# Kernel tuning notes

Hardware: AMD Instinct MI355X
Metric: run time of the kernel (lower is better)

The kernel has to match this reference:

```python
import jax, jax.numpy as jnp
import numpy as np

B, T = 4096, 512          # batch, max seq len
V, E, H, O = 57, 20, 128, 18  # vocab, embed, hidden, classes


def setup_inputs() -> dict:
    key = jax.random.key(0)
    ks = jax.random.split(key, 9)
    x = jax.random.randint(ks[0], (B, T), 0, V)
    lens = jax.random.randint(ks[1], (B,), 1, T + 1)
    x_lengths = jnp.sort(lens)[::-1]  # pack_padded_sequence needs descending lengths
    s = 1.0 / np.sqrt(H)
    emb = jax.random.normal(ks[2], (V, E), dtype=jnp.float32)
    W_ih = jax.random.uniform(ks[3], (H, E), minval=-s, maxval=s, dtype=jnp.float32)
    W_hh = jax.random.uniform(ks[4], (H, H), minval=-s, maxval=s, dtype=jnp.float32)
    b_ih = jax.random.uniform(ks[5], (H,), minval=-s, maxval=s, dtype=jnp.float32)
    b_hh = jax.random.uniform(ks[6], (H,), minval=-s, maxval=s, dtype=jnp.float32)
    so = 1.0 / np.sqrt(H)
    W_out = jax.random.uniform(ks[7], (O, H), minval=-so, maxval=so, dtype=jnp.float32)
    b_out = jax.random.uniform(ks[8], (O,), minval=-so, maxval=so, dtype=jnp.float32)
    return {"x": x, "x_lengths": x_lengths, "emb": emb, "W_ih": W_ih,
            "W_hh": W_hh, "b_ih": b_ih, "b_hh": b_hh, "W_out": W_out, "b_out": b_out}


def reference(x, x_lengths, emb, W_ih, W_hh, b_ih, b_hh, W_out, b_out):
    xe = emb[x]                                            # [B,T,E] embedding gather
    # precompute input projection + both biases once (hoisted out of recurrence)
    xw = jnp.einsum('bte,he->bth', xe, W_ih) + b_ih + b_hh  # [B,T,H]
    valid = jnp.arange(T)[None, :] < x_lengths[:, None]     # [B,T] packed-seq mask

    def step(h, inp):
        xw_t, v_t = inp                                     # [B,H], [B]
        h_new = jnp.tanh(xw_t + h @ W_hh.T)
        # packed RNN: stop updating once past this sequence's length,
        # so the final h equals the hidden state at step len-1
        h = jnp.where(v_t[:, None], h_new, h)
        return h, None

    h0 = jnp.zeros((B, H), dtype=xw.dtype)
    hT, _ = jax.lax.scan(step, h0, (jnp.swapaxes(xw, 0, 1), valid.T))  # scan over T
    logits = jax.nn.relu(hT) @ W_out.T + b_out              # [B,O]
    return jax.nn.log_softmax(logits, axis=1)
```

## Files before the change

kernel.cpp:

```cpp
#include <hip/hip_runtime.h>
#include <math.h>

#define Bn 4096
#define Tn 512
#define Vn 57
#define En 20
#define Hn 128
#define On 18
#define ROWS 16
#define NTHR 512
#define NBLK (Bn / ROWS)
#define KC 5
#define NKB 20
#define BUFH (NKB * 16 * 8)
#define ESTR 40
#define XSTR 513
#define HFSTR 132
#define ASCALE 2.8853900817779268f

typedef _Float16 half8  __attribute__((ext_vector_type(8)));
typedef _Float16 half4  __attribute__((ext_vector_type(4)));
typedef __fp16   fp16x2 __attribute__((ext_vector_type(2)));
typedef float    floatx4 __attribute__((ext_vector_type(4)));

__device__ __forceinline__ float tanh_scaled(float z) {
    float e = __builtin_amdgcn_exp2f(z);
    float r = __builtin_amdgcn_rcpf(e + 1.0f);
    return fmaf(-2.0f, r, 1.0f);
}

__device__ __forceinline__ unsigned pk_u32(fp16x2 v) {
    union { fp16x2 h; unsigned u; } c; c.h = v; return c.u;
}

__launch_bounds__(NTHR, 2)
__global__ void rnn_mfma_kernel(const int* __restrict__ x,
                                const int* __restrict__ xlen,
                                const float* __restrict__ emb,
                                const float* __restrict__ W_ih,
                                const float* __restrict__ W_hh,
                                const float* __restrict__ b_ih,
                                const float* __restrict__ b_hh,
                                const float* __restrict__ W_out,
                                const float* __restrict__ b_out,
                                float* __restrict__ out)
{
    __shared__ __align__(16) _Float16 sB[2][BUFH];
    __shared__ __align__(16) _Float16 sEmb[Vn * ESTR];
    __shared__ __align__(16) float    sHf[ROWS * HFSTR];
    __shared__ int sX[ROWS * XSTR];
    __shared__ float sLogit[ROWS][On];
    __shared__ float sMLS[ROWS];
    __shared__ float sPad[6200];

    const int tid  = threadIdx.x;
    const int blk  = blockIdx.x;
    const int row0 = blk * ROWS;

    ((volatile float*)sPad)[tid % 6200] = 0.0f;

    const int w    = tid >> 6;
    const int lane = tid & 63;
    const int n    = lane & 15;
    const int q    = lane >> 4;
    const bool stager = (w >= 4) && (lane < 16);
    const int  wk     = (w >= 4) ? (w - 4) : 0;

    half8 Ah[KC];
    #pragma unroll
    for (int kc = 0; kc < 4; ++kc) {
        const float* p = &W_hh[(16 * w + n) * Hn + kc * 32 + q * 8];
        #pragma unroll
        for (int i = 0; i < 8; ++i)
            Ah[kc][i] = (_Float16)(p[i] * ASCALE);
    }
    {
        #pragma unroll
        for (int i = 0; i < 8; ++i) {
            int e = q * 8 + i;
            float v = 0.0f;
            if (e < En)       v = W_ih[(16 * w + n) * En + e];
            else if (e == 20) v = b_ih[16 * w + n] + b_hh[16 * w + n];
            Ah[4][i] = (_Float16)(v * ASCALE);
        }
    }

    for (int idx = tid; idx < Vn * 32; idx += NTHR) {
        int c = idx >> 5, j = idx & 31;
        float v = (j < En) ? emb[c * En + j] : (j == 20 ? 1.0f : 0.0f);
        sEmb[c * ESTR + j] = (_Float16)v;
    }
    for (int idx = tid * 4; idx < ROWS * Tn; idx += NTHR * 4) {
        int4 v = *(const int4*)&x[row0 * Tn + idx];
        int r = idx >> 9, t = idx & 511;
        sX[r * XSTR + t]     = v.x;
        sX[r * XSTR + t + 1] = v.y;
        sX[r * XSTR + t + 2] = v.z;
        sX[r * XSTR + t + 3] = v.w;
    }
    for (int idx = tid; idx < 2 * BUFH / 8; idx += NTHR)
        ((float4*)sB)[idx] = make_float4(0.f, 0.f, 0.f, 0.f);
    __syncthreads();

    const int Lmax  = xlen[row0];
    const int len_n = xlen[row0 + n];

    if (stager) {
        int id0 = sX[lane * XSTR + 0];
        half8 xe0 = *(const half8*)&sEmb[id0 * ESTR + wk * 8];
        *(half8*)&sB[0][(16 + wk) * 128 + lane * 8] = xe0;
    }
    __syncthreads();

    float hreg[4] = {0.f, 0.f, 0.f, 0.f};

    const int bbase = q * 128 + n * 8;
    const int kbA   = 2 * w + (q >> 1);
    const int sadr  = kbA * 128 + n * 8 + 4 * (q & 1);

    int id_use = 0;
    if (stager) id_use = sX[lane * XSTR + (Lmax > 1 ? 1 : 0)];

    #define RNN_STEP(bp, np, t)                                                   \
    {                                                                             \
        half8 b[KC];                                                              \
        _Pragma("unroll")                                                         \
        for (int kc = 0; kc < KC; ++kc)                                           \
            b[kc] = *(const half8*)&(bp)[bbase + kc * 512];                       \
        half8 xe;                                                                 \
        int id_next = 0;                                                          \
        if (stager) {                                                             \
            xe = *(const half8*)&sEmb[id_use * ESTR + wk * 8];                    \
            id_next = sX[lane * XSTR + min((t) + 2, Lmax - 1)];                   \
        }                                                                         \
        floatx4 aE = {0.f, 0.f, 0.f, 0.f};                                        \
        floatx4 aO = {0.f, 0.f, 0.f, 0.f};                                        \
        aE = __builtin_amdgcn_mfma_f32_16x16x32_f16(Ah[0], b[0], aE, 0, 0, 0);    \
        aO = __builtin_amdgcn_mfma_f32_16x16x32_f16(Ah[1], b[1], aO, 0, 0, 0);    \
        aE = __builtin_amdgcn_mfma_f32_16x16x32_f16(Ah[2], b[2], aE, 0, 0, 0);    \
        aO = __builtin_amdgcn_mfma_f32_16x16x32_f16(Ah[3], b[3], aO, 0, 0, 0);    \
        aE = __builtin_amdgcn_mfma_f32_16x16x32_f16(Ah[4], b[4], aE, 0, 0, 0);    \
        const bool upd = ((t) < len_n);                                           \
        _Pragma("unroll")                                                         \
        for (int i = 0; i < 4; ++i) {                                             \
            float v = tanh_scaled(aE[i] + aO[i]);                                 \
            hreg[i] = upd ? v : hreg[i];                                          \
        }                                                                         \
        fp16x2 p0 = __builtin_amdgcn_cvt_pkrtz(hreg[0], hreg[1]);                 \
        fp16x2 p1 = __builtin_amdgcn_cvt_pkrtz(hreg[2], hreg[3]);                 \
        uint2 pk; pk.x = pk_u32(p0); pk.y = pk_u32(p1);                           \
        *(uint2*)&(np)[sadr] = pk;                                                \
        if (stager)                                                               \
            *(half8*)&(np)[(16 + wk) * 128 + lane * 8] = xe;                      \
        id_use = id_next;                                                         \
        __syncthreads();                                                          \
    }

    int t = 0;
    for (; t + 2 <= Lmax; t += 2) {
        RNN_STEP(&sB[0][0], &sB[1][0], t);
        RNN_STEP(&sB[1][0], &sB[0][0], t + 1);
    }
    if (t < Lmax) {
        RNN_STEP(&sB[0][0], &sB[1][0], t);
    }
    #undef RNN_STEP

    {
        float4 f0;
        f0.x = hreg[0]; f0.y = hreg[1]; f0.z = hreg[2]; f0.w = hreg[3];
        *(float4*)&sHf[n * HFSTR + 16 * w + 4 * q] = f0;
    }
    __syncthreads();

    for (int it = tid; it < ROWS * On; it += NTHR) {
        int r = it / On, c = it % On;
        float acc = b_out[c];
        for (int k = 0; k < Hn; ++k) {
            float hv = sHf[r * HFSTR + k];
            hv = hv > 0.0f ? hv : 0.0f;
            acc = fmaf(hv, W_out[c * Hn + k], acc);
        }
        sLogit[r][c] = acc;
    }
    __syncthreads();

    if (tid < ROWS) {
        float m = -INFINITY;
        #pragma unroll
        for (int c = 0; c < On; ++c) m = fmaxf(m, sLogit[tid][c]);
        float s = 0.0f;
        #pragma unroll
        for (int c = 0; c < On; ++c) s += __expf(sLogit[tid][c] - m);
        sMLS[tid] = m + __logf(s);
    }
    __syncthreads();

    for (int it = tid; it < ROWS * On; it += NTHR) {
        int r = it / On, c = it % On;
        out[(row0 + r) * On + c] = sLogit[r][c] - sMLS[r];
    }
}

extern "C" void kernel_launch(void* const* d_in, const int* in_sizes, int n_in,
                              void* d_out, int out_size, void* d_ws, size_t ws_size,
                              hipStream_t stream) {
    const int*   x     = (const int*)d_in[0];
    const int*   xlen  = (const int*)d_in[1];
    const float* emb   = (const float*)d_in[2];
    const float* W_ih  = (const float*)d_in[3];
    const float* W_hh  = (const float*)d_in[4];
    const float* b_ih  = (const float*)d_in[5];
    const float* b_hh  = (const float*)d_in[6];
    const float* W_out = (const float*)d_in[7];
    const float* b_out = (const float*)d_in[8];
    float*       out   = (float*)d_out;

    rnn_mfma_kernel<<<NBLK, NTHR, 0, stream>>>(x, xlen, emb, W_ih, W_hh,
                                               b_ih, b_hh, W_out, b_out, out);
}
```

Baseline: 233.7 us.

## Halve block to 4 waves, each computing 32 hidden units with permuted exchange layout

Block size drops from 8 to 4 waves, so each wave computes two 16-row MFMA tiles of W_hh (32 hidden units) and keeps double the A fragments in registers. Hidden rows are permuted so each lane's 8 outputs pack into one uint4 written straight into the B-fragment layout of a compact exchange buffer. Every lane now loads its own embedding fragment, which removes the dedicated stager lanes. The intent is cheaper per-step barriers with fewer waves and more MFMA work per wave to hide latency, at the cost of higher register pressure and a longer serial chain per wave.

```diff
diff --git a/kernel.cpp b/kernel.cpp
--- a/kernel.cpp
+++ b/kernel.cpp
@@ -8,18 +8,15 @@
 #define Hn 128
 #define On 18
 #define ROWS 16
-#define NTHR 512
+#define NTHR 256
 #define NBLK (Bn / ROWS)
 #define KC 5
-#define NKB 20
-#define BUFH (NKB * 16 * 8)
 #define ESTR 40
 #define XSTR 513
 #define HFSTR 132
 #define ASCALE 2.8853900817779268f
 
 typedef _Float16 half8  __attribute__((ext_vector_type(8)));
-typedef _Float16 half4  __attribute__((ext_vector_type(4)));
 typedef __fp16   fp16x2 __attribute__((ext_vector_type(2)));
 typedef float    floatx4 __attribute__((ext_vector_type(4)));
 
@@ -33,7 +30,7 @@
     union { fp16x2 h; unsigned u; } c; c.h = v; return c.u;
 }
 
-__launch_bounds__(NTHR, 2)
+__launch_bounds__(NTHR, 1)
 __global__ void rnn_mfma_kernel(const int* __restrict__ x,
                                 const int* __restrict__ xlen,
                                 const float* __restrict__ emb,
@@ -45,43 +42,44 @@
                                 const float* __restrict__ b_out,
                                 float* __restrict__ out)
 {
-    __shared__ __align__(16) _Float16 sB[2][BUFH];
+    __shared__ __align__(16) uint4    exB[2][4][64];
     __shared__ __align__(16) _Float16 sEmb[Vn * ESTR];
     __shared__ __align__(16) float    sHf[ROWS * HFSTR];
-    __shared__ int sX[ROWS * XSTR];
+    __shared__ int   sX[ROWS * XSTR];
     __shared__ float sLogit[ROWS][On];
     __shared__ float sMLS[ROWS];
-    __shared__ float sPad[6200];
+    __shared__ float sPad[6800];
 
     const int tid  = threadIdx.x;
     const int blk  = blockIdx.x;
     const int row0 = blk * ROWS;
 
-    ((volatile float*)sPad)[tid % 6200] = 0.0f;
+    ((volatile float*)sPad)[tid % 6800] = 0.0f;
 
     const int w    = tid >> 6;
     const int lane = tid & 63;
     const int n    = lane & 15;
     const int q    = lane >> 4;
-    const bool stager = (w >= 4) && (lane < 16);
-    const int  wk     = (w >= 4) ? (w - 4) : 0;
-
-    half8 Ah[KC];
+
+    half8 Ah[2][KC];
+    const int fA0 = 32 * w + 8 * (n >> 2) + (n & 3);
     #pragma unroll
-    for (int kc = 0; kc < 4; ++kc) {
-        const float* p = &W_hh[(16 * w + n) * Hn + kc * 32 + q * 8];
-        #pragma unroll
-        for (int i = 0; i < 8; ++i)
-            Ah[kc][i] = (_Float16)(p[i] * ASCALE);
-    }
-    {
+    for (int b = 0; b < 2; ++b) {
+        const int f = fA0 + 4 * b;
+        #pragma unroll
+        for (int kc = 0; kc < 4; ++kc) {
+            const float* p = &W_hh[f * Hn + kc * 32 + q * 8];
+            #pragma unroll
+            for (int i = 0; i < 8; ++i)
+                Ah[b][kc][i] = (_Float16)(p[i] * ASCALE);
+        }
         #pragma unroll
         for (int i = 0; i < 8; ++i) {
             int e = q * 8 + i;
             float v = 0.0f;
-            if (e < En)       v = W_ih[(16 * w + n) * En + e];
-            else if (e == 20) v = b_ih[16 * w + n] + b_hh[16 * w + n];
-            Ah[4][i] = (_Float16)(v * ASCALE);
+            if (e < En)       v = W_ih[f * En + e];
+            else if (e == 20) v = b_ih[f] + b_hh[f];
+            Ah[b][4][i] = (_Float16)(v * ASCALE);
         }
     }
 
@@ -98,78 +96,77 @@
         sX[r * XSTR + t + 2] = v.z;
         sX[r * XSTR + t + 3] = v.w;
     }
-    for (int idx = tid; idx < 2 * BUFH / 8; idx += NTHR)
-        ((float4*)sB)[idx] = make_float4(0.f, 0.f, 0.f, 0.f);
+    for (int idx = tid; idx < 2 * 4 * 64; idx += NTHR)
+        ((uint4*)exB)[idx] = make_uint4(0u, 0u, 0u, 0u);
     __syncthreads();
 
     const int Lmax  = xlen[row0];
     const int len_n = xlen[row0 + n];
 
-    if (stager) {
-        int id0 = sX[lane * XSTR + 0];
-        half8 xe0 = *(const half8*)&sEmb[id0 * ESTR + wk * 8];
-        *(half8*)&sB[0][(16 + wk) * 128 + lane * 8] = xe0;
-    }
-    __syncthreads();
-
-    float hreg[4] = {0.f, 0.f, 0.f, 0.f};
-
-    const int bbase = q * 128 + n * 8;
-    const int kbA   = 2 * w + (q >> 1);
-    const int sadr  = kbA * 128 + n * 8 + 4 * (q & 1);
-
-    int id_use = 0;
-    if (stager) id_use = sX[lane * XSTR + (Lmax > 1 ? 1 : 0)];
-
-    #define RNN_STEP(bp, np, t)                                                   \
+    int   idN;
+    half8 xeC;
+    {
+        int id0 = sX[n * XSTR];
+        xeC = *(const half8*)&sEmb[id0 * ESTR + 8 * q];
+        idN = sX[n * XSTR + (Lmax > 1 ? 1 : 0)];
+    }
+
+    float hreg[8] = {0.f, 0.f, 0.f, 0.f, 0.f, 0.f, 0.f, 0.f};
+
+    #define RNN_STEP(BR, BW, t)                                                   \
     {                                                                             \
-        half8 b[KC];                                                              \
-        _Pragma("unroll")                                                         \
-        for (int kc = 0; kc < KC; ++kc)                                           \
-            b[kc] = *(const half8*)&(bp)[bbase + kc * 512];                       \
-        half8 xe;                                                                 \
-        int id_next = 0;                                                          \
-        if (stager) {                                                             \
-            xe = *(const half8*)&sEmb[id_use * ESTR + wk * 8];                    \
-            id_next = sX[lane * XSTR + min((t) + 2, Lmax - 1)];                   \
-        }                                                                         \
-        floatx4 aE = {0.f, 0.f, 0.f, 0.f};                                        \
-        floatx4 aO = {0.f, 0.f, 0.f, 0.f};                                        \
-        aE = __builtin_amdgcn_mfma_f32_16x16x32_f16(Ah[0], b[0], aE, 0, 0, 0);    \
-        aO = __builtin_amdgcn_mfma_f32_16x16x32_f16(Ah[1], b[1], aO, 0, 0, 0);    \
-        aE = __builtin_amdgcn_mfma_f32_16x16x32_f16(Ah[2], b[2], aE, 0, 0, 0);    \
-        aO = __builtin_amdgcn_mfma_f32_16x16x32_f16(Ah[3], b[3], aO, 0, 0, 0);    \
-        aE = __builtin_amdgcn_mfma_f32_16x16x32_f16(Ah[4], b[4], aE, 0, 0, 0);    \
+        half8 bf0 = *(const half8*)&exB[BR][0][lane];                             \
+        half8 bf1 = *(const half8*)&exB[BR][1][lane];                             \
+        half8 bf2 = *(const half8*)&exB[BR][2][lane];                             \
+        half8 bf3 = *(const half8*)&exB[BR][3][lane];                             \
+        half8 xeN = *(const half8*)&sEmb[idN * ESTR + 8 * q];                     \
+        int idN2 = sX[n * XSTR + min((t) + 2, Lmax - 1)];                         \
+        floatx4 aE0 = {0.f,0.f,0.f,0.f}, aO0 = {0.f,0.f,0.f,0.f};                 \
+        floatx4 aE1 = {0.f,0.f,0.f,0.f}, aO1 = {0.f,0.f,0.f,0.f};                 \
+        aE0 = __builtin_amdgcn_mfma_f32_16x16x32_f16(Ah[0][0], bf0, aE0, 0,0,0);  \
+        aE1 = __builtin_amdgcn_mfma_f32_16x16x32_f16(Ah[1][0], bf0, aE1, 0,0,0);  \
+        aO0 = __builtin_amdgcn_mfma_f32_16x16x32_f16(Ah[0][1], bf1, aO0, 0,0,0);  \
+        aO1 = __builtin_amdgcn_mfma_f32_16x16x32_f16(Ah[1][1], bf1, aO1, 0,0,0);  \
+        aE0 = __builtin_amdgcn_mfma_f32_16x16x32_f16(Ah[0][2], bf2, aE0, 0,0,0);  \
+        aE1 = __builtin_amdgcn_mfma_f32_16x16x32_f16(Ah[1][2], bf2, aE1, 0,0,0);  \
+        aO0 = __builtin_amdgcn_mfma_f32_16x16x32_f16(Ah[0][3], bf3, aO0, 0,0,0);  \
+        aO1 = __builtin_amdgcn_mfma_f32_16x16x32_f16(Ah[1][3], bf3, aO1, 0,0,0);  \
+        aE0 = __builtin_amdgcn_mfma_f32_16x16x32_f16(Ah[0][4], xeC, aE0, 0,0,0);  \
+        aE1 = __builtin_amdgcn_mfma_f32_16x16x32_f16(Ah[1][4], xeC, aE1, 0,0,0);  \
         const bool upd = ((t) < len_n);                                           \
         _Pragma("unroll")                                                         \
         for (int i = 0; i < 4; ++i) {                                             \
-            float v = tanh_scaled(aE[i] + aO[i]);                                 \
-            hreg[i] = upd ? v : hreg[i];                                          \
+            float v0 = tanh_scaled(aE0[i] + aO0[i]);                              \
+            float v1 = tanh_scaled(aE1[i] + aO1[i]);                              \
+            hreg[i]     = upd ? v0 : hreg[i];                                     \
+            hreg[4 + i] = upd ? v1 : hreg[4 + i];                                 \
         }                                                                         \
-        fp16x2 p0 = __builtin_amdgcn_cvt_pkrtz(hreg[0], hreg[1]);                 \
-        fp16x2 p1 = __builtin_amdgcn_cvt_pkrtz(hreg[2], hreg[3]);                 \
-        uint2 pk; pk.x = pk_u32(p0); pk.y = pk_u32(p1);                           \
-        *(uint2*)&(np)[sadr] = pk;                                                \
-        if (stager)                                                               \
-            *(half8*)&(np)[(16 + wk) * 128 + lane * 8] = xe;                      \
-        id_use = id_next;                                                         \
+        uint4 pk;                                                                 \
+        pk.x = pk_u32(__builtin_amdgcn_cvt_pkrtz(hreg[0], hreg[1]));              \
+        pk.y = pk_u32(__builtin_amdgcn_cvt_pkrtz(hreg[2], hreg[3]));              \
+        pk.z = pk_u32(__builtin_amdgcn_cvt_pkrtz(hreg[4], hreg[5]));              \
+        pk.w = pk_u32(__builtin_amdgcn_cvt_pkrtz(hreg[6], hreg[7]));              \
+        exB[BW][w][lane] = pk;                                                    \
+        xeC = xeN; idN = idN2;                                                    \
         __syncthreads();                                                          \
     }
 
     int t = 0;
     for (; t + 2 <= Lmax; t += 2) {
-        RNN_STEP(&sB[0][0], &sB[1][0], t);
-        RNN_STEP(&sB[1][0], &sB[0][0], t + 1);
+        RNN_STEP(0, 1, t);
+        RNN_STEP(1, 0, t + 1);
     }
     if (t < Lmax) {
-        RNN_STEP(&sB[0][0], &sB[1][0], t);
+        RNN_STEP(0, 1, t);
     }
     #undef RNN_STEP
 
     {
-        float4 f0;
+        float4 f0, f1;
         f0.x = hreg[0]; f0.y = hreg[1]; f0.z = hreg[2]; f0.w = hreg[3];
-        *(float4*)&sHf[n * HFSTR + 16 * w + 4 * q] = f0;
+        f1.x = hreg[4]; f1.y = hreg[5]; f1.z = hreg[6]; f1.w = hreg[7];
+        *(float4*)&sHf[n * HFSTR + 32 * w + 8 * q]     = f0;
+        *(float4*)&sHf[n * HFSTR + 32 * w + 8 * q + 4] = f1;
     }
     __syncthreads();
 
```

Measured after the change: 288.3 us. +23.4%, slower.
